# Kernel tuning notes

Measured on AMD Instinct MI355X. Metric: run time of the kernel, lower is better.

The kernel has to match this reference:

```python
import jax, jax.numpy as jnp
import numpy as np


def setup_inputs() -> dict:
    key = jax.random.key(0)
    k1, k2 = jax.random.split(key)
    x = jax.random.normal(k1, (16, 512, 64, 64), dtype=jnp.float32)
    beta = jax.random.uniform(k2, (1,), dtype=jnp.float32)
    return {"x": x, "beta": beta}


def reference(x, beta):
    b, c, h, w = x.shape
    hw = h * w
    # F.avg_pool2d(x, kernel_size=2, stride=2)
    Fp = x.reshape(b, c, h // 2, 2, w // 2, 2).mean(axis=(3, 5))  # [b,c,h/2,w/2]
    F_flat = Fp.reshape(b, c, -1)                                  # [b,c,hw/4]
    # channel-channel attention
    Sc = jax.nn.softmax(jnp.einsum('bcn,bdn->bcd', F_flat, F_flat), axis=-1)  # [b,c,c]
    Mc = jnp.einsum('bcd,bdn->bcn', Sc, F_flat).reshape(b, c, h // 2, w // 2)
    # bilinear upsample, align_corners=False (half-pixel convention)
    Mc = jax.image.resize(Mc, (b, c, h, w), method='bilinear')
    A_flat = x.reshape(b, c, hw)
    Mc_flat = Mc.reshape(b, c, hw)
    Ac = A_flat - A_flat.mean(axis=-1, keepdims=True)
    Mcc = Mc_flat - Mc_flat.mean(axis=-1, keepdims=True)
    cov = jnp.einsum('bcn,bdn->bcd', Ac, Mcc) / hw                # [b,c,c]
    Lc = Sc + cov
    Ec = jnp.einsum('bcd,bdn->bcn', Lc, A_flat).reshape(b, c, h, w)
    attention_map = beta[0] * Ec + x
    out = x * attention_map
    return (out, cov, Sc, Ec)
```

## Files before the change

### kernel.cpp

```cpp
#include <hip/hip_runtime.h>
#include <hip/hip_bf16.h>

typedef unsigned short u16;
typedef __attribute__((ext_vector_type(8))) short bf16x8;
typedef __attribute__((ext_vector_type(4))) float f32x4;

#define BB 16
#define CCH 512
#define HW 4096
#define PP 1024

__device__ __forceinline__ u16 f2bf(float f) {
  union { float f; unsigned u; } v; v.f = f;
  unsigned r = v.u + 0x7fffu + ((v.u >> 16) & 1u);
  return (u16)(r >> 16);
}
__device__ __forceinline__ float bf2f(u16 h) {
  union { unsigned u; float f; } v; v.u = ((unsigned)h) << 16;
  return v.f;
}

typedef __attribute__((address_space(1))) const unsigned gas_u32;
typedef __attribute__((address_space(3))) unsigned las_u32;
__device__ __forceinline__ void gl_lds16(const u16* g, u16* l) {
  __builtin_amdgcn_global_load_lds((gas_u32*)g, (las_u32*)l, 16, 0, 0);
}

__global__ __launch_bounds__(256) void pool_kernel(
    const float* __restrict__ x, u16* __restrict__ Fb, u16* __restrict__ Xb,
    float* __restrict__ xmean) {
  int bc = blockIdx.x;
  const float4* xr4 = (const float4*)(x + (size_t)bc * HW);
  ushort4* xb4 = (ushort4*)(Xb + (size_t)bc * HW);
  ushort2* fb2 = (ushort2*)(Fb + (size_t)bc * PP);
  int t = threadIdx.x;
  float sum = 0.f;
#pragma unroll
  for (int s = 0; s < 2; ++s) {
    int i = s * 256 + t;
    int py = i >> 4, pxq = i & 15;
    float4 a = xr4[(2 * py) * 16 + pxq];
    float4 b = xr4[(2 * py + 1) * 16 + pxq];
    float p0 = 0.25f * (a.x + a.y + b.x + b.y);
    float p1 = 0.25f * (a.z + a.w + b.z + b.w);
    ushort2 fp; fp.x = f2bf(p0); fp.y = f2bf(p1);
    fb2[i] = fp;
    sum += p0 + p1;
    ushort4 ua; ua.x = f2bf(a.x); ua.y = f2bf(a.y); ua.z = f2bf(a.z); ua.w = f2bf(a.w);
    ushort4 ub; ub.x = f2bf(b.x); ub.y = f2bf(b.y); ub.z = f2bf(b.z); ub.w = f2bf(b.w);
    xb4[(2 * py) * 16 + pxq] = ua;
    xb4[(2 * py + 1) * 16 + pxq] = ub;
  }
#pragma unroll
  for (int o = 32; o; o >>= 1) sum += __shfl_xor(sum, o);
  __shared__ float red[4];
  if ((t & 63) == 0) red[t >> 6] = sum;
  __syncthreads();
  if (t == 0) xmean[bc] = (red[0] + red[1] + red[2] + red[3]) * (1.0f / 1024.0f);
}

__global__ __launch_bounds__(256) void transpose_bf16(
    const u16* __restrict__ in, u16* __restrict__ out, int R, int C) {
  __shared__ u16 t[64][65];
  size_t bo = (size_t)blockIdx.z * R * C;
  int tr = blockIdx.y * 64, tc = blockIdx.x * 64;
  int tid = threadIdx.x;
#pragma unroll
  for (int s = 0; s < 2; ++s) {
    int i = tid + s * 256;
    int r = i >> 3, c8 = (i & 7) * 8;
    bf16x8 v = *(const bf16x8*)&in[bo + (size_t)(tr + r) * C + tc + c8];
#pragma unroll
    for (int j = 0; j < 8; ++j) t[r][c8 + j] = (u16)v[j];
  }
  __syncthreads();
#pragma unroll
  for (int s = 0; s < 2; ++s) {
    int i = tid + s * 256;
    int n = i >> 3, k8 = (i & 7) * 8;
    bf16x8 o;
#pragma unroll
    for (int j = 0; j < 8; ++j) o[j] = (short)t[k8 + j][n];
    *(bf16x8*)&out[bo + (size_t)(tc + n) * R + tr + k8] = o;
  }
}

__global__ void softmax_rows(const float* __restrict__ P, float* __restrict__ Sc,
                             u16* __restrict__ S1b) {
  size_t row = blockIdx.x;
  int z = (int)(row >> 9);
  const float* p0 = P + ((size_t)z * 2) * 262144 + (size_t)(row & 511) * 512;
  const float* p1 = p0 + 262144;
  float* g = Sc + row * 512;
  int lane = threadIdx.x;
  float v[8];
  float mx = -3.4e38f;
#pragma unroll
  for (int i = 0; i < 8; ++i) {
    int d = lane + i * 64;
    v[i] = p0[d] + p1[d];
    mx = fmaxf(mx, v[i]);
  }
#pragma unroll
  for (int o = 32; o; o >>= 1) mx = fmaxf(mx, __shfl_xor(mx, o));
  float s = 0.f;
#pragma unroll
  for (int i = 0; i < 8; ++i) { v[i] = expf(v[i] - mx); s += v[i]; }
#pragma unroll
  for (int o = 32; o; o >>= 1) s += __shfl_xor(s, o);
  float inv = 1.0f / s;
  int c = (int)(row & 511);
#pragma unroll
  for (int i = 0; i < 8; ++i) {
    int d = lane + i * 64;
    float sc = v[i] * inv;
    g[d] = sc;
    S1b[row * 512 + d] = f2bf(sc - (d == c ? 1.0f : 0.0f));
  }
}

__global__ __launch_bounds__(256) void upsample_kernel(
    const u16* __restrict__ Mcb, u16* __restrict__ Mup, float* __restrict__ mmean) {
  __shared__ float lm[1024];
  __shared__ float red[4];
  size_t bd = blockIdx.x;
  const u16* src = Mcb + bd * 1024;
  u16* dst = Mup + bd * 4096;
  int tid = threadIdx.x;
  for (int i = tid; i < 1024; i += 256) lm[i] = bf2f(src[i]);
  __syncthreads();
  float sum = 0.f;
#pragma unroll
  for (int it = 0; it < 16; ++it) {
    int idx = it * 256 + tid;
    int oy = idx >> 6, ox = idx & 63;
    int jy = oy >> 1, jx = ox >> 1;
    int y0, y1; float wy0;
    if (oy & 1) { y0 = jy; y1 = (jy < 31) ? jy + 1 : 31; wy0 = 0.75f; }
    else        { y0 = (jy > 0) ? jy - 1 : 0; y1 = jy; wy0 = (oy == 0) ? 0.0f : 0.25f; }
    int x0, x1; float wx0;
    if (ox & 1) { x0 = jx; x1 = (jx < 31) ? jx + 1 : 31; wx0 = 0.75f; }
    else        { x0 = (jx > 0) ? jx - 1 : 0; x1 = jx; wx0 = (ox == 0) ? 0.0f : 0.25f; }
    float wy1 = 1.0f - wy0, wx1 = 1.0f - wx0;
    float v = wy0 * (wx0 * lm[y0 * 32 + x0] + wx1 * lm[y0 * 32 + x1])
            + wy1 * (wx0 * lm[y1 * 32 + x0] + wx1 * lm[y1 * 32 + x1]);
    sum += v;
    dst[idx] = f2bf(v);
  }
#pragma unroll
  for (int o = 32; o; o >>= 1) sum += __shfl_xor(sum, o);
  if ((tid & 63) == 0) red[tid >> 6] = sum;
  __syncthreads();
  if (tid == 0) mmean[bd] = (red[0] + red[1] + red[2] + red[3]) * (1.0f / 4096.0f);
}

template <int MODE, int LOGSPLIT>
__global__ __launch_bounds__(256) void gemm_nt(
    const u16* __restrict__ A, const u16* __restrict__ B, int K, int lda, int ldb,
    size_t aStride, size_t bStride,
    float* __restrict__ outF, float* __restrict__ out2F, u16* __restrict__ outB,
    const u16* __restrict__ addB, const float* __restrict__ addF,
    const float* __restrict__ bp, int ldo, size_t oStride) {
  __shared__ u16 As[128 * 32];
  __shared__ u16 Bs[128 * 32];
  const int tid = threadIdx.x;
  const int lane = tid & 63, wave = tid >> 6;
  const int wr = wave >> 1, wc = wave & 1;
  const int zi = blockIdx.z;
  const int sp = zi & ((1 << LOGSPLIT) - 1);
  const int z = zi >> LOGSPLIT;
  const u16* Ab = A + (size_t)z * aStride + (size_t)sp * K + (size_t)(blockIdx.y * 128) * lda;
  const u16* Bb = B + (size_t)z * bStride + (size_t)sp * K + (size_t)(blockIdx.x * 128) * ldb;

  f32x4 acc[4][4] = {};

  const int stRow = lane >> 2;
  const int stCol = (lane & 3) * 8;
  u16* aL0 = As + (wave * 16) * 32;
  u16* aL1 = As + ((wave + 4) * 16) * 32;
  u16* bL0 = Bs + (wave * 16) * 32;
  u16* bL1 = Bs + ((wave + 4) * 16) * 32;
  const int fr = lane & 15, kq = lane >> 4;

  for (int k0 = 0; k0 < K; k0 += 32) {
    __syncthreads();
    gl_lds16(Ab + (size_t)(wave * 16 + stRow) * lda + k0 + stCol, aL0);
    gl_lds16(Ab + (size_t)((wave + 4) * 16 + stRow) * lda + k0 + stCol, aL1);
    gl_lds16(Bb + (size_t)(wave * 16 + stRow) * ldb + k0 + stCol, bL0);
    gl_lds16(Bb + (size_t)((wave + 4) * 16 + stRow) * ldb + k0 + stCol, bL1);
    __syncthreads();
    bf16x8 af[4], bfr[4];
#pragma unroll
    for (int m = 0; m < 4; ++m)
      af[m] = *(const bf16x8*)&As[(wr * 64 + m * 16 + fr) * 32 + kq * 8];
#pragma unroll
    for (int n = 0; n < 4; ++n)
      bfr[n] = *(const bf16x8*)&Bs[(wc * 64 + n * 16 + fr) * 32 + kq * 8];
#pragma unroll
    for (int m = 0; m < 4; ++m)
#pragma unroll
      for (int n = 0; n < 4; ++n)
        acc[m][n] = __builtin_amdgcn_mfma_f32_16x16x32_bf16(af[m], bfr[n], acc[m][n], 0, 0, 0);
  }

  float betaV = 0.f;
  if constexpr (MODE == 4) betaV = bp[0];
  const int cq = lane >> 4, cr = lane & 15;
#pragma unroll
  for (int m = 0; m < 4; ++m) {
#pragma unroll
    for (int n = 0; n < 4; ++n) {
      int row0 = blockIdx.y * 128 + wr * 64 + m * 16 + cq * 4;
      int col  = blockIdx.x * 128 + wc * 64 + n * 16 + cr;
#pragma unroll
      for (int j = 0; j < 4; ++j) {
        int r = row0 + j;
        float val = acc[m][n][j];
        size_t idx = oStride * (size_t)zi + (size_t)r * ldo + col;
        if constexpr (MODE == 0) {
          outF[idx] = val;
        } else if constexpr (MODE == 1) {
          outB[idx] = f2bf(val + bf2f(addB[idx]));
        } else if constexpr (MODE == 3) {
          outF[idx] = val + addF[idx];
        } else if constexpr (MODE == 4) {
          float xv = addF[idx];
          float ec = val + xv;
          outF[idx] = ec;
          out2F[idx] = xv * (betaV * ec + xv);
        }
      }
    }
  }
}

__global__ __launch_bounds__(256) void combine_cov(
    const float* __restrict__ parts, const float* __restrict__ sc,
    const float* __restrict__ xm, const float* __restrict__ mm,
    float* __restrict__ cov, u16* __restrict__ L1b) {
  int row = blockIdx.x;
  int z = row >> 9, r = row & 511;
  size_t base = (size_t)z * 262144 + (size_t)r * 512;
  size_t pz = (size_t)z * 4 * 262144 + (size_t)r * 512;
  float xmr = xm[row];
#pragma unroll
  for (int j = 0; j < 2; ++j) {
    int c = threadIdx.x + j * 256;
    float s = parts[pz + c] + parts[pz + 262144 + c] +
              parts[pz + 2 * 262144 + c] + parts[pz + 3 * 262144 + c];
    float cv = s * (1.0f / 4096.0f) - xmr * mm[z * 512 + c];
    cov[base + c] = cv;
    L1b[base + c] = f2bf(sc[base + c] + cv - (r == c ? 1.0f : 0.0f));
  }
}

__global__ void finalize_kernel(const float* __restrict__ x, const float* __restrict__ ec,
                                const float* __restrict__ beta, float* __restrict__ out) {
  float b = beta[0];
  size_t i = (size_t)blockIdx.x * 256 + threadIdx.x;
  size_t stride = (size_t)gridDim.x * 256;
  const float4* x4 = (const float4*)x;
  const float4* e4 = (const float4*)ec;
  float4* o4 = (float4*)out;
  size_t n4 = (size_t)BB * CCH * HW / 4;
  for (size_t p = i; p < n4; p += stride) {
    float4 xv = x4[p], ev = e4[p];
    float4 ov;
    ov.x = xv.x * (b * ev.x + xv.x);
    ov.y = xv.y * (b * ev.y + xv.y);
    ov.z = xv.z * (b * ev.z + xv.z);
    ov.w = xv.w * (b * ev.w + xv.w);
    o4[p] = ov;
  }
}

extern "C" void kernel_launch(void* const* d_in, const int* in_sizes, int n_in,
                              void* d_out, int out_size, void* d_ws, size_t ws_size,
                              hipStream_t stream) {
  const float* x = (const float*)d_in[0];
  const float* beta = (const float*)d_in[1];

  const size_t NX = (size_t)BB * CCH * HW;
  const size_t NCOV = (size_t)BB * CCH * CCH;

  float* out_f = (float*)d_out;
  float* cov_f = out_f + NX;
  float* sc_f  = cov_f + NCOV;
  float* ec_f  = sc_f + NCOV;

  u16* Xb = (u16*)ec_f;
  float* spare = ec_f + NX / 2;

  char* w = (char*)d_ws;
  u16* Fb   = (u16*)(w);
  u16* FbT  = (u16*)(w + 16777216);
  u16* Mcb  = (u16*)(w + 33554432);
  u16* S1b  = (u16*)(w + 50331648);
  u16* L1b  = (u16*)(w + 58720256);
  float* xmean = (float*)(w + 67108864);
  float* mmean = (float*)(w + 67141632);
  const size_t WS_BASE = 67174400;
  const bool bigws = ws_size >= WS_BASE + (size_t)134217728;

  u16* XbT = bigws ? (u16*)(w + WS_BASE) : (u16*)d_out;
  u16* Mup = (u16*)d_out + NX;

  pool_kernel<<<BB * CCH, 256, 0, stream>>>(x, Fb, Xb, xmean);
  transpose_bf16<<<dim3(16, 8, BB), 256, 0, stream>>>(Fb, FbT, 512, 1024);
  transpose_bf16<<<dim3(64, 8, BB), 256, 0, stream>>>(Xb, XbT, 512, 4096);
  gemm_nt<0, 1><<<dim3(4, 4, BB * 2), 256, 0, stream>>>(
      Fb, Fb, 512, 1024, 1024, (size_t)CCH * PP, (size_t)CCH * PP,
      spare, nullptr, nullptr, nullptr, nullptr, nullptr, 512, 262144);
  softmax_rows<<<BB * CCH, 64, 0, stream>>>(spare, sc_f, S1b);
  gemm_nt<1, 0><<<dim3(8, 4, BB), 256, 0, stream>>>(
      S1b, FbT, 512, 512, 512, (size_t)CCH * CCH, (size_t)PP * CCH,
      nullptr, nullptr, Mcb, Fb, nullptr, nullptr, 1024, (size_t)CCH * PP);
  upsample_kernel<<<BB * CCH, 256, 0, stream>>>(Mcb, Mup, mmean);
  gemm_nt<0, 2><<<dim3(4, 4, BB * 4), 256, 0, stream>>>(
      Xb, Mup, 1024, 4096, 4096, NX / BB, NX / BB,
      spare, nullptr, nullptr, nullptr, nullptr, nullptr, 512, 262144);
  combine_cov<<<BB * CCH, 256, 0, stream>>>(spare, sc_f, xmean, mmean, cov_f, L1b);
  if (bigws) {
    gemm_nt<4, 0><<<dim3(32, 4, BB), 256, 0, stream>>>(
        L1b, XbT, 512, 512, 512, (size_t)CCH * CCH, NX / BB,
        ec_f, out_f, nullptr, nullptr, x, beta, 4096, NX / BB);
  } else {
    gemm_nt<3, 0><<<dim3(32, 4, BB), 256, 0, stream>>>(
        L1b, XbT, 512, 512, 512, (size_t)CCH * CCH, NX / BB,
        ec_f, nullptr, nullptr, nullptr, x, nullptr, 4096, NX / BB);
    finalize_kernel<<<4096, 256, 0, stream>>>(x, ec_f, beta, out_f);
  }
}
```

Measured before the change: 698.4 us.

## Move bilinear upsample onto x via adjoint, shrinking covariance GEMM K to 1024

The bilinear upsample is linear, so the covariance GEMM is rewritten as the adjoint of the upsample applied to x (computed in the pool kernel from an LDS-staged row) times the low-res Mc. This cuts the cov GEMM's K dimension from 4096 to 1024 and drops the upsample kernel and the Mup buffer. Mc's row mean now comes from a small kernel, since the upsample preserves the mean. A fused fp32-to-bf16 transpose of x replaces the bf16 copy plus its transpose. The pool kernel gains a 16KB LDS stage and clamped edge-weight arithmetic, and any mismatch in the adjoint edge handling would change the numerics.

Measured after the change: 609.6 us. 12.7% less time.

```diff
diff --git a/kernel.cpp b/kernel.cpp
--- a/kernel.cpp
+++ b/kernel.cpp
@@ -27,36 +27,82 @@
 }
 
 __global__ __launch_bounds__(256) void pool_kernel(
-    const float* __restrict__ x, u16* __restrict__ Fb, u16* __restrict__ Xb,
+    const float* __restrict__ x, u16* __restrict__ Fb, u16* __restrict__ XUb,
     float* __restrict__ xmean) {
+  __shared__ float row[4096];
+  __shared__ float red[4];
   int bc = blockIdx.x;
   const float4* xr4 = (const float4*)(x + (size_t)bc * HW);
-  ushort4* xb4 = (ushort4*)(Xb + (size_t)bc * HW);
-  ushort2* fb2 = (ushort2*)(Fb + (size_t)bc * PP);
+  float4* r4 = (float4*)row;
   int t = threadIdx.x;
+#pragma unroll
+  for (int s = 0; s < 4; ++s) r4[t + s * 256] = xr4[t + s * 256];
+  __syncthreads();
+  ushort2* f2 = (ushort2*)(Fb + (size_t)bc * PP);
+  ushort2* u2 = (ushort2*)(XUb + (size_t)bc * PP);
   float sum = 0.f;
 #pragma unroll
   for (int s = 0; s < 2; ++s) {
     int i = s * 256 + t;
     int py = i >> 4, pxq = i & 15;
-    float4 a = xr4[(2 * py) * 16 + pxq];
-    float4 b = xr4[(2 * py + 1) * 16 + pxq];
-    float p0 = 0.25f * (a.x + a.y + b.x + b.y);
-    float p1 = 0.25f * (a.z + a.w + b.z + b.w);
+    const float* r0 = row + (2 * py) * 64;
+    const float* r1 = r0 + 64;
+    int c0 = 4 * pxq;
+    float p0 = 0.25f * (r0[c0] + r0[c0 + 1] + r1[c0] + r1[c0 + 1]);
+    float p1 = 0.25f * (r0[c0 + 2] + r0[c0 + 3] + r1[c0 + 2] + r1[c0 + 3]);
     ushort2 fp; fp.x = f2bf(p0); fp.y = f2bf(p1);
-    fb2[i] = fp;
+    f2[i] = fp;
     sum += p0 + p1;
-    ushort4 ua; ua.x = f2bf(a.x); ua.y = f2bf(a.y); ua.z = f2bf(a.z); ua.w = f2bf(a.w);
-    ushort4 ub; ub.x = f2bf(b.x); ub.y = f2bf(b.y); ub.z = f2bf(b.z); ub.w = f2bf(b.w);
-    xb4[(2 * py) * 16 + pxq] = ua;
-    xb4[(2 * py + 1) * 16 + pxq] = ub;
+    int ry0 = (py == 0) ? 0 : 2 * py - 1;
+    int ry3 = (py == 31) ? 63 : 2 * py + 2;
+    const float* ra = row + ry0 * 64;
+    const float* rd = row + ry3 * 64;
+    float rm[6];
+#pragma unroll
+    for (int k = 0; k < 6; ++k) {
+      int c = 4 * pxq - 1 + k;
+      c = c < 0 ? 0 : (c > 63 ? 63 : c);
+      rm[k] = 0.25f * (ra[c] + rd[c]) + 0.75f * (r0[c] + r1[c]);
+    }
+    float xu0 = 0.25f * (rm[0] + rm[3]) + 0.75f * (rm[1] + rm[2]);
+    float xu1 = 0.25f * (rm[2] + rm[5]) + 0.75f * (rm[3] + rm[4]);
+    ushort2 up; up.x = f2bf(xu0); up.y = f2bf(xu1);
+    u2[i] = up;
   }
 #pragma unroll
   for (int o = 32; o; o >>= 1) sum += __shfl_xor(sum, o);
-  __shared__ float red[4];
   if ((t & 63) == 0) red[t >> 6] = sum;
   __syncthreads();
   if (t == 0) xmean[bc] = (red[0] + red[1] + red[2] + red[3]) * (1.0f / 1024.0f);
+}
+
+__global__ __launch_bounds__(256) void transpose_x_bf16(
+    const float* __restrict__ in, u16* __restrict__ out) {
+  __shared__ u16 t[64][65];
+  int b = blockIdx.z;
+  const float* ib = in + (size_t)b * CCH * HW;
+  u16* ob = out + (size_t)b * HW * CCH;
+  int tr = blockIdx.y * 64;
+  int tc = blockIdx.x * 64;
+  int tid = threadIdx.x;
+#pragma unroll
+  for (int s = 0; s < 4; ++s) {
+    int i = tid + s * 256;
+    int r = i >> 4, c4 = (i & 15) * 4;
+    float4 v = *(const float4*)&ib[(size_t)(tr + r) * HW + tc + c4];
+    t[r][c4] = f2bf(v.x); t[r][c4 + 1] = f2bf(v.y);
+    t[r][c4 + 2] = f2bf(v.z); t[r][c4 + 3] = f2bf(v.w);
+  }
+  __syncthreads();
+#pragma unroll
+  for (int s = 0; s < 2; ++s) {
+    int i = tid + s * 256;
+    int n = i >> 3, k8 = (i & 7) * 8;
+    bf16x8 o;
+#pragma unroll
+    for (int j = 0; j < 8; ++j) o[j] = (short)t[k8 + j][n];
+    *(bf16x8*)&ob[(size_t)(tc + n) * CCH + tr + k8] = o;
+  }
 }
 
 __global__ __launch_bounds__(256) void transpose_bf16(
@@ -119,39 +165,17 @@
   }
 }
 
-__global__ __launch_bounds__(256) void upsample_kernel(
-    const u16* __restrict__ Mcb, u16* __restrict__ Mup, float* __restrict__ mmean) {
-  __shared__ float lm[1024];
-  __shared__ float red[4];
-  size_t bd = blockIdx.x;
-  const u16* src = Mcb + bd * 1024;
-  u16* dst = Mup + bd * 4096;
-  int tid = threadIdx.x;
-  for (int i = tid; i < 1024; i += 256) lm[i] = bf2f(src[i]);
-  __syncthreads();
-  float sum = 0.f;
-#pragma unroll
-  for (int it = 0; it < 16; ++it) {
-    int idx = it * 256 + tid;
-    int oy = idx >> 6, ox = idx & 63;
-    int jy = oy >> 1, jx = ox >> 1;
-    int y0, y1; float wy0;
-    if (oy & 1) { y0 = jy; y1 = (jy < 31) ? jy + 1 : 31; wy0 = 0.75f; }
-    else        { y0 = (jy > 0) ? jy - 1 : 0; y1 = jy; wy0 = (oy == 0) ? 0.0f : 0.25f; }
-    int x0, x1; float wx0;
-    if (ox & 1) { x0 = jx; x1 = (jx < 31) ? jx + 1 : 31; wx0 = 0.75f; }
-    else        { x0 = (jx > 0) ? jx - 1 : 0; x1 = jx; wx0 = (ox == 0) ? 0.0f : 0.25f; }
-    float wy1 = 1.0f - wy0, wx1 = 1.0f - wx0;
-    float v = wy0 * (wx0 * lm[y0 * 32 + x0] + wx1 * lm[y0 * 32 + x1])
-            + wy1 * (wx0 * lm[y1 * 32 + x0] + wx1 * lm[y1 * 32 + x1]);
-    sum += v;
-    dst[idx] = f2bf(v);
-  }
-#pragma unroll
-  for (int o = 32; o; o >>= 1) sum += __shfl_xor(sum, o);
-  if ((tid & 63) == 0) red[tid >> 6] = sum;
-  __syncthreads();
-  if (tid == 0) mmean[bd] = (red[0] + red[1] + red[2] + red[3]) * (1.0f / 4096.0f);
+__global__ void mc_rowmean(const u16* __restrict__ Mcb, float* __restrict__ mmean) {
+  int row = blockIdx.x;
+  const bf16x8* src = (const bf16x8*)(Mcb + (size_t)row * PP);
+  int lane = threadIdx.x;
+  bf16x8 v0 = src[lane], v1 = src[lane + 64];
+  float s = 0.f;
+#pragma unroll
+  for (int j = 0; j < 8; ++j) s += bf2f((u16)v0[j]) + bf2f((u16)v1[j]);
+#pragma unroll
+  for (int o = 32; o; o >>= 1) s += __shfl_xor(s, o);
+  if (lane == 0) mmean[row] = s * (1.0f / 1024.0f);
 }
 
 template <int MODE, int LOGSPLIT>
@@ -241,13 +265,12 @@
   int row = blockIdx.x;
   int z = row >> 9, r = row & 511;
   size_t base = (size_t)z * 262144 + (size_t)r * 512;
-  size_t pz = (size_t)z * 4 * 262144 + (size_t)r * 512;
+  size_t pz = (size_t)z * 2 * 262144 + (size_t)r * 512;
   float xmr = xm[row];
 #pragma unroll
   for (int j = 0; j < 2; ++j) {
     int c = threadIdx.x + j * 256;
-    float s = parts[pz + c] + parts[pz + 262144 + c] +
-              parts[pz + 2 * 262144 + c] + parts[pz + 3 * 262144 + c];
+    float s = parts[pz + c] + parts[pz + 262144 + c];
     float cv = s * (1.0f / 4096.0f) - xmr * mm[z * 512 + c];
     cov[base + c] = cv;
     L1b[base + c] = f2bf(sc[base + c] + cv - (r == c ? 1.0f : 0.0f));
@@ -282,32 +305,32 @@
 
   const size_t NX = (size_t)BB * CCH * HW;
   const size_t NCOV = (size_t)BB * CCH * CCH;
+  const size_t MB = 1u << 20;
 
   float* out_f = (float*)d_out;
   float* cov_f = out_f + NX;
   float* sc_f  = cov_f + NCOV;
   float* ec_f  = sc_f + NCOV;
 
-  u16* Xb = (u16*)ec_f;
-  float* spare = ec_f + NX / 2;
+  float* spare = ec_f;
 
   char* w = (char*)d_ws;
   u16* Fb   = (u16*)(w);
-  u16* FbT  = (u16*)(w + 16777216);
-  u16* Mcb  = (u16*)(w + 33554432);
-  u16* S1b  = (u16*)(w + 50331648);
-  u16* L1b  = (u16*)(w + 58720256);
-  float* xmean = (float*)(w + 67108864);
-  float* mmean = (float*)(w + 67141632);
-  const size_t WS_BASE = 67174400;
-  const bool bigws = ws_size >= WS_BASE + (size_t)134217728;
+  u16* FbT  = (u16*)(w + 16 * MB);
+  u16* Mcb  = (u16*)(w + 32 * MB);
+  u16* XUb  = (u16*)(w + 48 * MB);
+  u16* S1b  = (u16*)(w + 64 * MB);
+  u16* L1b  = (u16*)(w + 72 * MB);
+  float* xmean = (float*)(w + 80 * MB);
+  float* mmean = (float*)(w + 80 * MB + 65536);
+  const size_t WS_BASE = 81 * MB;
+  const bool bigws = ws_size >= WS_BASE + 64 * MB;
 
   u16* XbT = bigws ? (u16*)(w + WS_BASE) : (u16*)d_out;
-  u16* Mup = (u16*)d_out + NX;
-
-  pool_kernel<<<BB * CCH, 256, 0, stream>>>(x, Fb, Xb, xmean);
+
+  pool_kernel<<<BB * CCH, 256, 0, stream>>>(x, Fb, XUb, xmean);
+  transpose_x_bf16<<<dim3(64, 8, BB), 256, 0, stream>>>(x, XbT);
   transpose_bf16<<<dim3(16, 8, BB), 256, 0, stream>>>(Fb, FbT, 512, 1024);
-  transpose_bf16<<<dim3(64, 8, BB), 256, 0, stream>>>(Xb, XbT, 512, 4096);
   gemm_nt<0, 1><<<dim3(4, 4, BB * 2), 256, 0, stream>>>(
       Fb, Fb, 512, 1024, 1024, (size_t)CCH * PP, (size_t)CCH * PP,
       spare, nullptr, nullptr, nullptr, nullptr, nullptr, 512, 262144);
@@ -315,14 +338,14 @@
   gemm_nt<1, 0><<<dim3(8, 4, BB), 256, 0, stream>>>(
       S1b, FbT, 512, 512, 512, (size_t)CCH * CCH, (size_t)PP * CCH,
       nullptr, nullptr, Mcb, Fb, nullptr, nullptr, 1024, (size_t)CCH * PP);
-  upsample_kernel<<<BB * CCH, 256, 0, stream>>>(Mcb, Mup, mmean);
-  gemm_nt<0, 2><<<dim3(4, 4, BB * 4), 256, 0, stream>>>(
-      Xb, Mup, 1024, 4096, 4096, NX / BB, NX / BB,
+  mc_rowmean<<<BB * CCH, 64, 0, stream>>>(Mcb, mmean);
+  gemm_nt<0, 1><<<dim3(4, 4, BB * 2), 256, 0, stream>>>(
+      XUb, Mcb, 512, 1024, 1024, (size_t)CCH * PP, (size_t)CCH * PP,
       spare, nullptr, nullptr, nullptr, nullptr, nullptr, 512, 262144);
   combine_cov<<<BB * CCH, 256, 0, stream>>>(spare, sc_f, xmean, mmean, cov_f, L1b);
   if (bigws) {
     gemm_nt<4, 0><<<dim3(32, 4, BB), 256, 0, stream>>>(
-        L1b, XbT, 512, 512, 512, (size_t)CCH * CCH, NX / BB,
+        L1b, XbT, 512, 512, 512, (size_t)CCH * CCH, (size_t)HW * CCH,
         ec_f, out_f, nullptr, nullptr, x, beta, 4096, NX / BB);
   } else {
     gemm_nt<3, 0><<<dim3(32, 4, BB), 256, 0, stream>>>(
```
